# Kernel tuning notes

Hardware: AMD Instinct MI355X
Metric: run time of the kernel (lower is better)

Reference implementation:

```python
import jax, jax.numpy as jnp
import numpy as np


def setup_inputs() -> dict:
    key = jax.random.key(0)
    k0, k1, k2, k3, k4 = jax.random.split(key, 5)
    feat0 = jax.random.normal(k0, (32, 256, 56, 56), dtype=jnp.float32)
    feat1 = jax.random.normal(k1, (32, 512, 28, 28), dtype=jnp.float32)
    feat2 = jax.random.normal(k2, (32, 1024, 14, 14), dtype=jnp.float32)
    feat3 = jax.random.normal(k3, (32, 2048, 7, 7), dtype=jnp.float32)
    # Conv2d(3840 -> 1024, kernel_size=1, bias=False): weight [emb, C_total]
    conv_w = jax.random.normal(k4, (1024, 3840), dtype=jnp.float32) * 0.02
    return {"feat0": feat0, "feat1": feat1, "feat2": feat2, "feat3": feat3, "conv_w": conv_w}


def reference(feat0, feat1, feat2, feat3, conv_w):
    # Target spatial size = earliest (largest) level.
    Ht, Wt = feat0.shape[2], feat0.shape[3]

    def up_mean(f):
        # Bilinear upsample (torch Upsample align_corners=False == jax 'bilinear'
        # half-pixel resize), then spatial mean per channel.  Because the 1x1
        # conv and global avg-pool are linear, pooling each upsampled level
        # first and applying the conv on the pooled vector is exactly the
        # same math as conv(concat(upsampled)) followed by avg-pool.
        B, C = f.shape[0], f.shape[1]
        up = jax.image.resize(f, (B, C, Ht, Wt), method='bilinear')  # [B,C,Ht,Wt]
        return jnp.mean(up, axis=(2, 3))  # [B,C]

    v = jnp.concatenate([up_mean(f) for f in (feat0, feat1, feat2, feat3)], axis=1)  # [B, 3840]
    # 1x1 conv (no bias) on pooled vector == GEMM with conv weight, then squeeze.
    return v @ conv_w.T  # [B, emb]
```

## Files before the change

### kernel.cpp

```cpp
#include <hip/hip_runtime.h>


__device__ __forceinline__ float s4(float4 a) { return (a.x + a.y) + (a.z + a.w); }

__global__ __launch_bounds__(256) void pool_kernel(
    const float* __restrict__ f0, const float* __restrict__ f1,
    const float* __restrict__ f2, const float* __restrict__ f3,
    float* __restrict__ v)
{
    int t = threadIdx.x, w = t >> 6, lane = t & 63;
    int bid = blockIdx.x;

    if (bid < 3072) {
        int chunk = bid * 4 + w;
        const float* base = (chunk < 8192)
            ? f0 + (size_t)chunk * 3136
            : f1 + (size_t)(chunk - 8192) * 3136;
        const float4* p = (const float4*)base;
        float4 r[12];
        #pragma unroll
        for (int i = 0; i < 12; ++i) r[i] = p[lane + (i << 6)];
        float4 tl = make_float4(0.f, 0.f, 0.f, 0.f);
        if (lane < 16) tl = p[768 + lane];

        if (chunk < 8192) {
            float s = 0.f;
            #pragma unroll
            for (int i = 0; i < 12; ++i) s += s4(r[i]);
            s += s4(tl);
            #pragma unroll
            for (int o = 32; o; o >>= 1) s += __shfl_xor(s, o);
            if (lane == 0)
                v[(chunk >> 8) * 3840 + (chunk & 255)] = s * (1.f / 3136.f);
        } else {
            float a0 = s4(r[0]) + s4(r[1]) + s4(r[2]) + (lane <  4 ? s4(r[3]) : 0.f);
            float a1 = (lane <  4 ? 0.f : s4(r[3])) + s4(r[4]) + s4(r[5])
                     + (lane <  8 ? s4(r[6]) : 0.f);
            float a2 = (lane <  8 ? 0.f : s4(r[6])) + s4(r[7]) + s4(r[8])
                     + (lane < 12 ? s4(r[9]) : 0.f);
            float a3 = (lane < 12 ? 0.f : s4(r[9])) + s4(r[10]) + s4(r[11]) + s4(tl);
            #pragma unroll
            for (int o = 32; o; o >>= 1) {
                a0 += __shfl_xor(a0, o); a1 += __shfl_xor(a1, o);
                a2 += __shfl_xor(a2, o); a3 += __shfl_xor(a3, o);
            }
            if (lane == 0) {
                int q = (chunk - 8192) * 4;
                float4 res = make_float4(a0, a1, a2, a3);
                *(float4*)&v[(q >> 9) * 3840 + 256 + (q & 511)] =
                    make_float4(res.x * (1.f / 784.f), res.y * (1.f / 784.f),
                                res.z * (1.f / 784.f), res.w * (1.f / 784.f));
            }
        }
    } else {
        int seg = (bid - 3072) * 256 + t;
        const float* sp = (seg < 131072)
            ? f2 + (size_t)seg * 49
            : f3 + (size_t)(seg - 131072) * 49;
        float x[49];
        #pragma unroll
        for (int i = 0; i < 49; ++i) x[i] = sp[i];
        float s = 0.f;
        #pragma unroll
        for (int i = 0; i < 48; i += 2) s += x[i] + x[i + 1];
        s += x[48];
        if (seg < 131072) {
            s += __shfl_xor(s, 1); s += __shfl_xor(s, 2);
            if ((lane & 3) == 0) {
                int q = seg >> 2;
                v[(q >> 10) * 3840 + 768 + (q & 1023)] = s * (1.f / 196.f);
            }
        } else {
            int q = seg - 131072;
            v[(q >> 11) * 3840 + 1792 + (q & 2047)] = s * (1.f / 49.f);
        }
    }
}

#define KT 120

__global__ __launch_bounds__(256) void gemm_kernel(
    const float* __restrict__ v, const float* __restrict__ W,
    float* __restrict__ partials)
{
    __shared__ float vs[32][124];
    __shared__ float wsh[64][124];
    int t = threadIdx.x;
    int et = blockIdx.x & 15, ks = blockIdx.x >> 4;
    int e0 = et << 6, k0 = ks * KT;

    {
        float4 tmp[7];
        int row[7], c4[7];
        #pragma unroll
        for (int i = 0; i < 7; ++i) {
            int f = t + (i << 8);
            row[i] = f / 30; c4[i] = f % 30;
            tmp[i] = *(const float4*)&W[(size_t)(e0 + row[i]) * 3840 + k0 + c4[i] * 4];
        }
        float4 tail; int rowt = 0, c4t = 0;
        if (t < 128) {
            int f = t + 1792;
            rowt = f / 30; c4t = f % 30;
            tail = *(const float4*)&W[(size_t)(e0 + rowt) * 3840 + k0 + c4t * 4];
        }
        #pragma unroll
        for (int i = 0; i < 7; ++i)
            *(float4*)&wsh[row[i]][c4[i] * 4] = tmp[i];
        if (t < 128)
            *(float4*)&wsh[rowt][c4t * 4] = tail;
    }
    {
        float4 tmp[3];
        int row[3], c4[3];
        #pragma unroll
        for (int i = 0; i < 3; ++i) {
            int f = t + (i << 8);
            row[i] = f / 30; c4[i] = f % 30;
            tmp[i] = *(const float4*)&v[row[i] * 3840 + k0 + c4[i] * 4];
        }
        float4 tail; int rowt = 0, c4t = 0;
        if (t < 192) {
            int f = t + 768;
            rowt = f / 30; c4t = f % 30;
            tail = *(const float4*)&v[rowt * 3840 + k0 + c4t * 4];
        }
        #pragma unroll
        for (int i = 0; i < 3; ++i)
            *(float4*)&vs[row[i]][c4[i] * 4] = tmp[i];
        if (t < 192)
            *(float4*)&vs[rowt][c4t * 4] = tail;
    }
    __syncthreads();

    int bg = t >> 5, eg = t & 31;
    int b0 = bg << 2;
    float acc[4][2] = {};
    #pragma unroll 5
    for (int k = 0; k < KT; k += 4) {
        float4 vv[4], ww[2];
        #pragma unroll
        for (int i = 0; i < 4; ++i) vv[i] = *(const float4*)&vs[b0 + i][k];
        #pragma unroll
        for (int j = 0; j < 2; ++j) ww[j] = *(const float4*)&wsh[eg + (j << 5)][k];
        #pragma unroll
        for (int i = 0; i < 4; ++i)
            #pragma unroll
            for (int j = 0; j < 2; ++j)
                acc[i][j] += vv[i].x * ww[j].x + vv[i].y * ww[j].y +
                             vv[i].z * ww[j].z + vv[i].w * ww[j].w;
    }

    float* pout = partials + (size_t)ks * 32768 + (size_t)b0 * 1024 + e0 + eg;
    #pragma unroll
    for (int i = 0; i < 4; ++i)
        #pragma unroll
        for (int j = 0; j < 2; ++j)
            pout[i * 1024 + (j << 5)] = acc[i][j];
}

__global__ __launch_bounds__(256) void reduce_kernel(
    const float* __restrict__ partials, float* __restrict__ out)
{
    int idx = blockIdx.x * 256 + threadIdx.x;
    float s0 = 0.f, s1 = 0.f, s2 = 0.f, s3 = 0.f;
    #pragma unroll
    for (int sp = 0; sp < 32; sp += 4) {
        s0 += partials[(sp + 0) * 32768 + idx];
        s1 += partials[(sp + 1) * 32768 + idx];
        s2 += partials[(sp + 2) * 32768 + idx];
        s3 += partials[(sp + 3) * 32768 + idx];
    }
    out[idx] = (s0 + s1) + (s2 + s3);
}

extern "C" void kernel_launch(void* const* d_in, const int* in_sizes, int n_in,
                              void* d_out, int out_size, void* d_ws, size_t ws_size,
                              hipStream_t stream)
{
    const float* f0 = (const float*)d_in[0];
    const float* f1 = (const float*)d_in[1];
    const float* f2 = (const float*)d_in[2];
    const float* f3 = (const float*)d_in[3];
    const float* W  = (const float*)d_in[4];
    float* out = (float*)d_out;

    float* v        = (float*)d_ws;
    float* partials = v + 32 * 3840;

    pool_kernel<<<3840, 256, 0, stream>>>(f0, f1, f2, f3, v);
    gemm_kernel<<<512, 256, 0, stream>>>(v, W, partials);
    reduce_kernel<<<128, 256, 0, stream>>>(partials, out);
}
```

Baseline: 234.2 us.

## Split pooling kernel; double-buffer large-level loads and stage small levels via LDS

The single pooling kernel becomes two. In the first, each wave reduces four 3136-float chunks of the two large levels, alternating between two register buffers so the next chunk's loads are in flight while the current one is reduced. In the second, each block copies a contiguous 50 KB tile of the small levels into shared memory with coalesced float4 loads, and threads then sum 49-element segments from LDS instead of doing strided per-thread global loads. This targets memory-bandwidth efficiency on a pass over roughly 200 MB, at the cost of one extra launch, higher register pressure, and lower occupancy from the large LDS footprint.

After: 239.7 us. +2.3%, slower.

```diff
diff --git a/kernel.cpp b/kernel.cpp
--- a/kernel.cpp
+++ b/kernel.cpp
@@ -3,77 +3,123 @@
 
 __device__ __forceinline__ float s4(float4 a) { return (a.x + a.y) + (a.z + a.w); }
 
-__global__ __launch_bounds__(256) void pool_kernel(
+__device__ __forceinline__ void loadc(float4 (&r)[13], const float4* __restrict__ p, int lane)
+{
+    #pragma unroll
+    for (int i = 0; i < 12; ++i) r[i] = p[lane + (i << 6)];
+    r[12] = make_float4(0.f, 0.f, 0.f, 0.f);
+    if (lane < 16) r[12] = p[768 + lane];
+}
+
+__device__ __forceinline__ float red_f0(const float4 (&r)[13])
+{
+    float s = 0.f;
+    #pragma unroll
+    for (int i = 0; i < 13; ++i) s += s4(r[i]);
+    #pragma unroll
+    for (int o = 32; o; o >>= 1) s += __shfl_xor(s, o);
+    return s;
+}
+
+__device__ __forceinline__ float4 red_f1(const float4 (&r)[13], int lane)
+{
+    float a0 = s4(r[0]) + s4(r[1]) + s4(r[2]) + (lane <  4 ? s4(r[3]) : 0.f);
+    float a1 = (lane <  4 ? 0.f : s4(r[3])) + s4(r[4]) + s4(r[5])
+             + (lane <  8 ? s4(r[6]) : 0.f);
+    float a2 = (lane <  8 ? 0.f : s4(r[6])) + s4(r[7]) + s4(r[8])
+             + (lane < 12 ? s4(r[9]) : 0.f);
+    float a3 = (lane < 12 ? 0.f : s4(r[9])) + s4(r[10]) + s4(r[11]) + s4(r[12]);
+    #pragma unroll
+    for (int o = 32; o; o >>= 1) {
+        a0 += __shfl_xor(a0, o); a1 += __shfl_xor(a1, o);
+        a2 += __shfl_xor(a2, o); a3 += __shfl_xor(a3, o);
+    }
+    return make_float4(a0, a1, a2, a3);
+}
+
+__device__ __forceinline__ void store_f1(float* __restrict__ v, int c, float4 a, int lane)
+{
+    if (lane == 0) {
+        int q = (c - 8192) * 4;
+        const float inv = 1.f / 784.f;
+        *(float4*)&v[(q >> 9) * 3840 + 256 + (q & 511)] =
+            make_float4(a.x * inv, a.y * inv, a.z * inv, a.w * inv);
+    }
+}
+
+__global__ __launch_bounds__(256) void pool_a_kernel(
     const float* __restrict__ f0, const float* __restrict__ f1,
+    float* __restrict__ v)
+{
+    int t = threadIdx.x, w = t >> 6, lane = t & 63;
+    int gw = (blockIdx.x << 2) | w;
+    int c0 = gw << 2;
+
+    const float4* p = (c0 < 8192)
+        ? (const float4*)(f0 + (size_t)c0 * 3136)
+        : (const float4*)(f1 + (size_t)(c0 - 8192) * 3136);
+
+    float4 ra[13], rb[13];
+    loadc(ra, p, lane);
+    loadc(rb, p + 784, lane);
+
+    if (c0 < 8192) {
+        float s0 = red_f0(ra); loadc(ra, p + 1568, lane);
+        float s1 = red_f0(rb); loadc(rb, p + 2352, lane);
+        float s2 = red_f0(ra);
+        float s3 = red_f0(rb);
+        float val = (lane == 0) ? s0 : (lane == 1) ? s1 : (lane == 2) ? s2 : s3;
+        if (lane < 4)
+            v[(c0 >> 8) * 3840 + (c0 & 255) + lane] = val * (1.f / 3136.f);
+    } else {
+        float4 a;
+        a = red_f1(ra, lane); loadc(ra, p + 1568, lane);
+        store_f1(v, c0 + 0, a, lane);
+        a = red_f1(rb, lane); loadc(rb, p + 2352, lane);
+        store_f1(v, c0 + 1, a, lane);
+        a = red_f1(ra, lane);
+        store_f1(v, c0 + 2, a, lane);
+        a = red_f1(rb, lane);
+        store_f1(v, c0 + 3, a, lane);
+    }
+}
+
+__global__ __launch_bounds__(256) void pool_bc_kernel(
     const float* __restrict__ f2, const float* __restrict__ f3,
     float* __restrict__ v)
 {
-    int t = threadIdx.x, w = t >> 6, lane = t & 63;
-    int bid = blockIdx.x;
-
-    if (bid < 3072) {
-        int chunk = bid * 4 + w;
-        const float* base = (chunk < 8192)
-            ? f0 + (size_t)chunk * 3136
-            : f1 + (size_t)(chunk - 8192) * 3136;
-        const float4* p = (const float4*)base;
-        float4 r[12];
-        #pragma unroll
-        for (int i = 0; i < 12; ++i) r[i] = p[lane + (i << 6)];
-        float4 tl = make_float4(0.f, 0.f, 0.f, 0.f);
-        if (lane < 16) tl = p[768 + lane];
-
-        if (chunk < 8192) {
-            float s = 0.f;
-            #pragma unroll
-            for (int i = 0; i < 12; ++i) s += s4(r[i]);
-            s += s4(tl);
-            #pragma unroll
-            for (int o = 32; o; o >>= 1) s += __shfl_xor(s, o);
-            if (lane == 0)
-                v[(chunk >> 8) * 3840 + (chunk & 255)] = s * (1.f / 3136.f);
-        } else {
-            float a0 = s4(r[0]) + s4(r[1]) + s4(r[2]) + (lane <  4 ? s4(r[3]) : 0.f);
-            float a1 = (lane <  4 ? 0.f : s4(r[3])) + s4(r[4]) + s4(r[5])
-                     + (lane <  8 ? s4(r[6]) : 0.f);
-            float a2 = (lane <  8 ? 0.f : s4(r[6])) + s4(r[7]) + s4(r[8])
-                     + (lane < 12 ? s4(r[9]) : 0.f);
-            float a3 = (lane < 12 ? 0.f : s4(r[9])) + s4(r[10]) + s4(r[11]) + s4(tl);
-            #pragma unroll
-            for (int o = 32; o; o >>= 1) {
-                a0 += __shfl_xor(a0, o); a1 += __shfl_xor(a1, o);
-                a2 += __shfl_xor(a2, o); a3 += __shfl_xor(a3, o);
-            }
-            if (lane == 0) {
-                int q = (chunk - 8192) * 4;
-                float4 res = make_float4(a0, a1, a2, a3);
-                *(float4*)&v[(q >> 9) * 3840 + 256 + (q & 511)] =
-                    make_float4(res.x * (1.f / 784.f), res.y * (1.f / 784.f),
-                                res.z * (1.f / 784.f), res.w * (1.f / 784.f));
-            }
+    __shared__ float4 ls4[3136];
+    float* ls = (float*)ls4;
+    int t = threadIdx.x, bid = blockIdx.x;
+
+    const float4* pp = (bid < 512)
+        ? (const float4*)(f2 + (size_t)bid * 12544)
+        : (const float4*)(f3 + (size_t)(bid - 512) * 12544);
+    #pragma unroll
+    for (int i = 0; i < 12; ++i) ls4[t + (i << 8)] = pp[t + (i << 8)];
+    if (t < 64) ls4[3072 + t] = pp[3072 + t];
+    __syncthreads();
+
+    if (bid < 512) {
+        int pl = t >> 2, q = t & 3;
+        const float* sp = ls + pl * 196 + q * 49;
+        float s = 0.f;
+        #pragma unroll
+        for (int i = 0; i < 48; i += 2) s += sp[i] + sp[i + 1];
+        s += sp[48];
+        s += __shfl_xor(s, 1); s += __shfl_xor(s, 2);
+        if (q == 0) {
+            int P = bid * 64 + pl;
+            v[(P >> 10) * 3840 + 768 + (P & 1023)] = s * (1.f / 196.f);
         }
     } else {
-        int seg = (bid - 3072) * 256 + t;
-        const float* sp = (seg < 131072)
-            ? f2 + (size_t)seg * 49
-            : f3 + (size_t)(seg - 131072) * 49;
-        float x[49];
-        #pragma unroll
-        for (int i = 0; i < 49; ++i) x[i] = sp[i];
+        const float* sp = ls + t * 49;
         float s = 0.f;
         #pragma unroll
-        for (int i = 0; i < 48; i += 2) s += x[i] + x[i + 1];
-        s += x[48];
-        if (seg < 131072) {
-            s += __shfl_xor(s, 1); s += __shfl_xor(s, 2);
-            if ((lane & 3) == 0) {
-                int q = seg >> 2;
-                v[(q >> 10) * 3840 + 768 + (q & 1023)] = s * (1.f / 196.f);
-            }
-        } else {
-            int q = seg - 131072;
-            v[(q >> 11) * 3840 + 1792 + (q & 2047)] = s * (1.f / 49.f);
-        }
+        for (int i = 0; i < 48; i += 2) s += sp[i] + sp[i + 1];
+        s += sp[48];
+        int P = (bid - 512) * 256 + t;
+        v[(P >> 11) * 3840 + 1792 + (P & 2047)] = s * (1.f / 49.f);
     }
 }
 
@@ -188,7 +234,8 @@
     float* v        = (float*)d_ws;
     float* partials = v + 32 * 3840;
 
-    pool_kernel<<<3840, 256, 0, stream>>>(f0, f1, f2, f3, v);
+    pool_a_kernel<<<768, 256, 0, stream>>>(f0, f1, v);
+    pool_bc_kernel<<<768, 256, 0, stream>>>(f2, f3, v);
     gemm_kernel<<<512, 256, 0, stream>>>(v, W, partials);
     reduce_kernel<<<128, 256, 0, stream>>>(partials, out);
 }
```
